# Kernel optimization log

Measured on AMD Instinct MI355X. Metric: run time of the kernel, lower is better.

Reference implementation:

```python
import jax, jax.numpy as jnp
import numpy as np

B, N = 4096, 8192
_BISECT_ITERS = 50


def _bisect_tau(z, u, iters=_BISECT_ITERS):
    """Find tau s.t. sum(clip(z - tau, 0, u)) == 1, per row. Returns tau [B,1]
    and region masks r1 (free: 0 < p < u) and r2 (saturated: p == u)."""
    lo = jnp.min(z - u, axis=-1, keepdims=True)   # f(lo) = sum(u) >= 1
    hi = jnp.max(z, axis=-1, keepdims=True)       # f(hi) = 0

    def body(_, lh):
        lo, hi = lh
        mid = 0.5 * (lo + hi)
        f = jnp.sum(jnp.clip(z - mid, 0.0, u), axis=-1, keepdims=True)
        too_big = f > 1.0
        return (jnp.where(too_big, mid, lo), jnp.where(too_big, hi, mid))

    lo, hi = jax.lax.fori_loop(0, iters, body, (lo, hi))
    tau = 0.5 * (lo + hi)
    d = z - tau
    r1 = (d > 0.0) & (d < u)   # interior / free coordinates
    r2 = d >= u                # clipped at upper bound u
    return tau, r1, r2


def setup_inputs() -> dict:
    key = jax.random.key(0)
    k1, k2 = jax.random.split(key)
    input1 = jax.random.normal(k1, (B, N), dtype=jnp.float32)
    input2 = jax.random.uniform(k2, (B, N), dtype=jnp.float32)
    return {"input1": input1, "input2": input2}


def reference(input1, input2):
    z, u = input1, input2
    tau0, r1, r2 = _bisect_tau(z, u)
    r1f = r1.astype(z.dtype)
    r2f = r2.astype(z.dtype)
    nA = jnp.sum(r1f, axis=-1, keepdims=True)  # size of free set
    # Exact tau from the identified active set (one Newton/KKT refinement):
    #   sum_{free}(z - tau) + sum_{sat} u = 1
    tau = (jnp.sum(r1f * z, axis=-1, keepdims=True)
           + jnp.sum(r2f * u, axis=-1, keepdims=True) - 1.0) / jnp.maximum(nA, 1.0)
    tau = jnp.where(nA > 0, tau, tau0)
    probs = r1f * (z - tau) + r2f * u
    return probs
```

## Files before the change

kernel.cpp:

```cpp
#include <hip/hip_runtime.h>


#define NCOLS   8192
#define THREADS 256
#define CHUNKS  8
#define ITERS   36

__device__ __forceinline__ float wsum(float v) {
#pragma unroll
  for (int o = 32; o > 0; o >>= 1) v += __shfl_xor(v, o, 64);
  return v;
}
__device__ __forceinline__ float wmin(float v) {
#pragma unroll
  for (int o = 32; o > 0; o >>= 1) v = fminf(v, __shfl_xor(v, o, 64));
  return v;
}
__device__ __forceinline__ float wmax(float v) {
#pragma unroll
  for (int o = 32; o > 0; o >>= 1) v = fmaxf(v, __shfl_xor(v, o, 64));
  return v;
}

__global__ __launch_bounds__(THREADS, 4) void csparsemax_kernel(
    const float* __restrict__ zg, const float* __restrict__ ug,
    float* __restrict__ og) {
  const int row  = blockIdx.x;
  const int tid  = threadIdx.x;
  const int wave = tid >> 6;
  const int lane = tid & 63;

  const float4* zp = (const float4*)(zg + (size_t)row * NCOLS);
  const float4* up = (const float4*)(ug + (size_t)row * NCOLS);
  float4*       op = (float4*)(og + (size_t)row * NCOLS);

  float4 z[CHUNKS], u[CHUNKS];
#pragma unroll
  for (int j = 0; j < CHUNKS; ++j) {
    z[j] = zp[tid + j * THREADS];
    u[j] = up[tid + j * THREADS];
  }

  __shared__ float lsum[2][4];
  __shared__ float lmm[8];
  __shared__ float l3[4][3];

  float lmin = 3.4e38f, lmax = -3.4e38f;
#pragma unroll
  for (int j = 0; j < CHUNKS; ++j) {
    lmin = fminf(lmin, fminf(fminf(z[j].x - u[j].x, z[j].y - u[j].y),
                             fminf(z[j].z - u[j].z, z[j].w - u[j].w)));
    lmax = fmaxf(lmax, fmaxf(fmaxf(z[j].x, z[j].y), fmaxf(z[j].z, z[j].w)));
  }
  lmin = wmin(lmin);
  lmax = wmax(lmax);
  if (lane == 0) { lmm[wave] = lmin; lmm[4 + wave] = lmax; }
  __syncthreads();
  float lo = fminf(fminf(lmm[0], lmm[1]), fminf(lmm[2], lmm[3]));
  float hi = fmaxf(fmaxf(lmm[4], lmm[5]), fmaxf(lmm[6], lmm[7]));

#pragma unroll 1
  for (int it = 0; it < ITERS; ++it) {
    float mid = 0.5f * (lo + hi);
    float s0 = 0.f, s1 = 0.f, s2 = 0.f, s3 = 0.f;
#pragma unroll
    for (int j = 0; j < CHUNKS; ++j) {
      s0 += __builtin_amdgcn_fmed3f(z[j].x - mid, 0.f, u[j].x);
      s1 += __builtin_amdgcn_fmed3f(z[j].y - mid, 0.f, u[j].y);
      s2 += __builtin_amdgcn_fmed3f(z[j].z - mid, 0.f, u[j].z);
      s3 += __builtin_amdgcn_fmed3f(z[j].w - mid, 0.f, u[j].w);
    }
    float s = wsum((s0 + s1) + (s2 + s3));
    if (lane == 0) lsum[it & 1][wave] = s;
    __syncthreads();
    float f = (lsum[it & 1][0] + lsum[it & 1][1]) +
              (lsum[it & 1][2] + lsum[it & 1][3]);
    if (f > 1.0f) lo = mid; else hi = mid;
  }

  float tau = 0.5f * (lo + hi);

#pragma unroll 1
  for (int r = 0; r < 2; ++r) {
    float cnt = 0.f, sz = 0.f, su = 0.f;
#pragma unroll
    for (int j = 0; j < CHUNKS; ++j) {
#define REFINE(c)                                          \
      {                                                    \
        float d  = z[j].c - tau;                           \
        bool  b1 = (d > 0.f) & (d < u[j].c);               \
        bool  b2 = d >= u[j].c;                            \
        cnt += b1 ? 1.f : 0.f;                             \
        sz  += b1 ? z[j].c : 0.f;                          \
        su  += b2 ? u[j].c : 0.f;                          \
      }
      REFINE(x) REFINE(y) REFINE(z) REFINE(w)
#undef REFINE
    }
    cnt = wsum(cnt); sz = wsum(sz); su = wsum(su);
    __syncthreads();
    if (lane == 0) { l3[wave][0] = cnt; l3[wave][1] = sz; l3[wave][2] = su; }
    __syncthreads();
    float nA = l3[0][0] + l3[1][0] + l3[2][0] + l3[3][0];
    float SZ = l3[0][1] + l3[1][1] + l3[2][1] + l3[3][1];
    float SU = l3[0][2] + l3[1][2] + l3[2][2] + l3[3][2];
    float nt = (SZ + SU - 1.0f) / fmaxf(nA, 1.0f);
    tau = (nA > 0.f) ? nt : tau;
  }

#pragma unroll
  for (int j = 0; j < CHUNKS; ++j) {
    float4 o;
    o.x = __builtin_amdgcn_fmed3f(z[j].x - tau, 0.f, u[j].x);
    o.y = __builtin_amdgcn_fmed3f(z[j].y - tau, 0.f, u[j].y);
    o.z = __builtin_amdgcn_fmed3f(z[j].z - tau, 0.f, u[j].z);
    o.w = __builtin_amdgcn_fmed3f(z[j].w - tau, 0.f, u[j].w);
    op[tid + j * THREADS] = o;
  }
}

extern "C" void kernel_launch(void* const* d_in, const int* in_sizes, int n_in,
                              void* d_out, int out_size, void* d_ws, size_t ws_size,
                              hipStream_t stream) {
  const float* z = (const float*)d_in[0];
  const float* u = (const float*)d_in[1];
  float*     out = (float*)d_out;
  const int rows = out_size / NCOLS;
  csparsemax_kernel<<<rows, THREADS, 0, stream>>>(z, u, out);
}
```

Measured before the change: 335.6 us.

## Compact bracket-active elements to LDS and finish bisection on one wave

After a few full-row bisection steps, the kernel classifies each element as saturated, inactive or still undetermined within the current bracket. Saturated sums are folded into a constant, and undetermined elements are appended to a shared-memory list through an atomic counter. A single wave then runs the remaining bisection and refinement over that small list instead of the whole row, cutting per-iteration work and block barriers. If the list overflows its capacity, the kernel falls back to full-row iterations. The cost is extra LDS use that may lower occupancy, plus LDS atomic contention.

```diff
diff --git a/kernel.cpp b/kernel.cpp
--- a/kernel.cpp
+++ b/kernel.cpp
@@ -4,7 +4,9 @@
 #define NCOLS   8192
 #define THREADS 256
 #define CHUNKS  8
-#define ITERS   36
+#define K1      8
+#define TAILI   30
+#define CAP     1024
 
 __device__ __forceinline__ float wsum(float v) {
 #pragma unroll
@@ -34,16 +36,26 @@
   const float4* up = (const float4*)(ug + (size_t)row * NCOLS);
   float4*       op = (float4*)(og + (size_t)row * NCOLS);
 
-  float4 z[CHUNKS], u[CHUNKS];
-#pragma unroll
-  for (int j = 0; j < CHUNKS; ++j) {
-    z[j] = zp[tid + j * THREADS];
-    u[j] = up[tid + j * THREADS];
-  }
-
   __shared__ float lsum[2][4];
   __shared__ float lmm[8];
   __shared__ float l3[4][3];
+  __shared__ float za[CAP], ua[CAP];
+  __shared__ int   scnt;
+  __shared__ float stau;
+
+  if (tid == 0) scnt = 0;
+
+  float4 z[CHUNKS], u[CHUNKS];
+#pragma unroll
+  for (int j = 0; j < CHUNKS; ++j) {
+    z[j] = zp[tid + j * THREADS];
+    u[j] = up[tid + j * THREADS];
+  }
+#pragma unroll
+  for (int j = 0; j < CHUNKS; ++j) {
+    asm volatile("" : "+v"(z[j].x), "+v"(z[j].y), "+v"(z[j].z), "+v"(z[j].w),
+                      "+v"(u[j].x), "+v"(u[j].y), "+v"(u[j].z), "+v"(u[j].w));
+  }
 
   float lmin = 3.4e38f, lmax = -3.4e38f;
 #pragma unroll
@@ -60,7 +72,7 @@
   float hi = fmaxf(fmaxf(lmm[4], lmm[5]), fmaxf(lmm[6], lmm[7]));
 
 #pragma unroll 1
-  for (int it = 0; it < ITERS; ++it) {
+  for (int it = 0; it < K1; ++it) {
     float mid = 0.5f * (lo + hi);
     float s0 = 0.f, s1 = 0.f, s2 = 0.f, s3 = 0.f;
 #pragma unroll
@@ -78,34 +90,113 @@
     if (f > 1.0f) lo = mid; else hi = mid;
   }
 
-  float tau = 0.5f * (lo + hi);
-
-#pragma unroll 1
-  for (int r = 0; r < 2; ++r) {
-    float cnt = 0.f, sz = 0.f, su = 0.f;
-#pragma unroll
-    for (int j = 0; j < CHUNKS; ++j) {
+  const float lo_c = lo, hi_c = hi;
+  float su = 0.f;
+#pragma unroll
+  for (int j = 0; j < CHUNKS; ++j) {
+#define CLASSIFY(c)                                          \
+    {                                                        \
+      float zz = z[j].c, uu = u[j].c;                        \
+      float d  = zz - uu;                                    \
+      bool  sat = d >= hi_c;                                 \
+      bool  act = (zz > lo_c) && (d < hi_c);                 \
+      su += sat ? uu : 0.f;                                  \
+      if (act) {                                             \
+        int k = atomicAdd(&scnt, 1);                         \
+        if (k < CAP) { za[k] = zz; ua[k] = uu; }             \
+      }                                                      \
+    }
+    CLASSIFY(x) CLASSIFY(y) CLASSIFY(z) CLASSIFY(w)
+#undef CLASSIFY
+  }
+  su = wsum(su);
+  if (lane == 0) lmm[wave] = su;
+  __syncthreads();
+  const float su_base = (lmm[0] + lmm[1]) + (lmm[2] + lmm[3]);
+  const int cnt = scnt;
+
+  float tau;
+  if (cnt <= CAP) {
+    if (wave == 0) {
+      float tlo = lo, thi = hi;
+#pragma unroll 1
+      for (int it = 0; it < TAILI; ++it) {
+        float mid = 0.5f * (tlo + thi);
+        float p = 0.f;
+        for (int k = lane; k < cnt; k += 64)
+          p += __builtin_amdgcn_fmed3f(za[k] - mid, 0.f, ua[k]);
+        float f = su_base + wsum(p);
+        if (f > 1.0f) tlo = mid; else thi = mid;
+      }
+      float t = 0.5f * (tlo + thi);
+#pragma unroll 1
+      for (int r = 0; r < 2; ++r) {
+        float c = 0.f, sz = 0.f, s2 = 0.f;
+        for (int k = lane; k < cnt; k += 64) {
+          float d  = za[k] - t;
+          bool  b1 = (d > 0.f) & (d < ua[k]);
+          bool  b2 = d >= ua[k];
+          c  += b1 ? 1.f : 0.f;
+          sz += b1 ? za[k] : 0.f;
+          s2 += b2 ? ua[k] : 0.f;
+        }
+        c  = wsum(c);
+        sz = wsum(sz);
+        s2 = wsum(s2) + su_base;
+        float nt = (sz + s2 - 1.0f) / fmaxf(c, 1.0f);
+        t = (c > 0.f) ? nt : t;
+      }
+      if (lane == 0) stau = t;
+    }
+    __syncthreads();
+    tau = stau;
+  } else {
+#pragma unroll 1
+    for (int it = K1; it < K1 + TAILI; ++it) {
+      float mid = 0.5f * (lo + hi);
+      float s0 = 0.f, s1 = 0.f, s2 = 0.f, s3 = 0.f;
+#pragma unroll
+      for (int j = 0; j < CHUNKS; ++j) {
+        s0 += __builtin_amdgcn_fmed3f(z[j].x - mid, 0.f, u[j].x);
+        s1 += __builtin_amdgcn_fmed3f(z[j].y - mid, 0.f, u[j].y);
+        s2 += __builtin_amdgcn_fmed3f(z[j].z - mid, 0.f, u[j].z);
+        s3 += __builtin_amdgcn_fmed3f(z[j].w - mid, 0.f, u[j].w);
+      }
+      float s = wsum((s0 + s1) + (s2 + s3));
+      if (lane == 0) lsum[it & 1][wave] = s;
+      __syncthreads();
+      float f = (lsum[it & 1][0] + lsum[it & 1][1]) +
+                (lsum[it & 1][2] + lsum[it & 1][3]);
+      if (f > 1.0f) lo = mid; else hi = mid;
+    }
+    tau = 0.5f * (lo + hi);
+#pragma unroll 1
+    for (int r = 0; r < 2; ++r) {
+      float cnt2 = 0.f, sz = 0.f, su2 = 0.f;
+#pragma unroll
+      for (int j = 0; j < CHUNKS; ++j) {
 #define REFINE(c)                                          \
-      {                                                    \
-        float d  = z[j].c - tau;                           \
-        bool  b1 = (d > 0.f) & (d < u[j].c);               \
-        bool  b2 = d >= u[j].c;                            \
-        cnt += b1 ? 1.f : 0.f;                             \
-        sz  += b1 ? z[j].c : 0.f;                          \
-        su  += b2 ? u[j].c : 0.f;                          \
-      }
-      REFINE(x) REFINE(y) REFINE(z) REFINE(w)
+        {                                                  \
+          float d  = z[j].c - tau;                         \
+          bool  b1 = (d > 0.f) & (d < u[j].c);             \
+          bool  b2 = d >= u[j].c;                          \
+          cnt2 += b1 ? 1.f : 0.f;                          \
+          sz   += b1 ? z[j].c : 0.f;                       \
+          su2  += b2 ? u[j].c : 0.f;                       \
+        }
+        REFINE(x) REFINE(y) REFINE(z) REFINE(w)
 #undef REFINE
-    }
-    cnt = wsum(cnt); sz = wsum(sz); su = wsum(su);
-    __syncthreads();
-    if (lane == 0) { l3[wave][0] = cnt; l3[wave][1] = sz; l3[wave][2] = su; }
-    __syncthreads();
-    float nA = l3[0][0] + l3[1][0] + l3[2][0] + l3[3][0];
-    float SZ = l3[0][1] + l3[1][1] + l3[2][1] + l3[3][1];
-    float SU = l3[0][2] + l3[1][2] + l3[2][2] + l3[3][2];
-    float nt = (SZ + SU - 1.0f) / fmaxf(nA, 1.0f);
-    tau = (nA > 0.f) ? nt : tau;
+      }
+      cnt2 = wsum(cnt2); sz = wsum(sz); su2 = wsum(su2);
+      __syncthreads();
+      if (lane == 0) { l3[wave][0] = cnt2; l3[wave][1] = sz; l3[wave][2] = su2; }
+      __syncthreads();
+      float nA = l3[0][0] + l3[1][0] + l3[2][0] + l3[3][0];
+      float SZ = l3[0][1] + l3[1][1] + l3[2][1] + l3[3][1];
+      float SU = l3[0][2] + l3[1][2] + l3[2][2] + l3[3][2];
+      float nt = (SZ + SU - 1.0f) / fmaxf(nA, 1.0f);
+      tau = (nA > 0.f) ? nt : tau;
+    }
   }
 
 #pragma unroll
```

Measured after the change: 322.2 us. -4.0%, faster.
